# Kernel optimization log

Measured on AMD Instinct MI355X. Metric: run time of the kernel, lower is better.

Reference implementation:

```python
import jax, jax.numpy as jnp
import numpy as np

NOISE_DIM = 32
HIDDEN_DIM = 256
DATA_DIM = 2
TEMP = 0.05
N = 16384
DIAG_PENALTY = 1e6


def _cdist(a, b):
    # Euclidean pairwise distance [Na, Nb], safe sqrt (zero grad at d==0 like torch.cdist)
    d2 = (jnp.sum(a * a, -1)[:, None] + jnp.sum(b * b, -1)[None, :]
          - 2.0 * (a @ b.T))
    d2 = jnp.maximum(d2, 0.0)
    safe = jnp.where(d2 > 0, d2, 1.0)
    return jnp.where(d2 > 0, jnp.sqrt(safe), 0.0)


def setup_inputs() -> dict:
    key = jax.random.key(0)
    ks = jax.random.split(key, 12)
    pos = jax.random.normal(ks[0], (N, DATA_DIM), dtype=jnp.float32)
    z = jax.random.normal(ks[1], (N, NOISE_DIM), dtype=jnp.float32)
    def lin(k, fan_in, fan_out):
        bound = 1.0 / np.sqrt(fan_in)
        k1, k2 = jax.random.split(k)
        W = jax.random.uniform(k1, (fan_in, fan_out), minval=-bound, maxval=bound, dtype=jnp.float32)
        b = jax.random.uniform(k2, (fan_out,), minval=-bound, maxval=bound, dtype=jnp.float32)
        return W, b
    W1, b1 = lin(ks[2], NOISE_DIM, HIDDEN_DIM)
    W2, b2 = lin(ks[3], HIDDEN_DIM, HIDDEN_DIM)
    W3, b3 = lin(ks[4], HIDDEN_DIM, HIDDEN_DIM)
    W4, b4 = lin(ks[5], HIDDEN_DIM, HIDDEN_DIM)
    W5, b5 = lin(ks[6], HIDDEN_DIM, DATA_DIM)
    return {"pos": pos, "z": z, "W1": W1, "b1": b1, "W2": W2, "b2": b2,
            "W3": W3, "b3": b3, "W4": W4, "b4": b4, "W5": W5, "b5": b5}


def reference(pos, z, W1, b1, W2, b2, W3, b3, W4, b4, W5, b5):
    # SELU MLP generator
    h = jax.nn.selu(z @ W1 + b1)
    h = jax.nn.selu(h @ W2 + b2)
    h = jax.nn.selu(h @ W3 + b3)
    h = jax.nn.selu(h @ W4 + b4)
    gen = h @ W5 + b5  # [N, D]

    y_pos = jax.lax.stop_gradient(pos)
    y_neg = jax.lax.stop_gradient(gen)

    dist_pos = _cdist(gen, y_pos)  # [N, N]
    dist_neg = _cdist(gen, y_neg)  # [N, N]
    dist_neg = dist_neg + jnp.eye(gen.shape[0], dtype=gen.dtype) * DIAG_PENALTY

    energy_pos = -TEMP * jax.nn.logsumexp(-dist_pos / TEMP, axis=1)
    energy_neg = TEMP * jax.nn.logsumexp(-dist_neg / TEMP, axis=1)
    return energy_pos + energy_neg  # [N]
```

## Files before the change

kernel.cpp:

```cpp
#include <hip/hip_runtime.h>
#include <hip/hip_bf16.h>

#define N_PTS 16384
#define TEMP_F 0.05f

__device__ __forceinline__ float selu_f(float x) {
    const float scale = 1.0507009873554805f;
    const float alpha = 1.6732632423543772f;
    return x > 0.f ? scale * x : scale * alpha * (__expf(x) - 1.f);
}

__device__ __forceinline__ float fast_sqrtf(float x) {
#if __has_builtin(__builtin_amdgcn_sqrtf)
    return __builtin_amdgcn_sqrtf(x);
#else
    return sqrtf(x);
#endif
}

__device__ __forceinline__ float fast_exp2f(float x) {
#if __has_builtin(__builtin_amdgcn_exp2f)
    return __builtin_amdgcn_exp2f(x);
#else
    return exp2f(x);
#endif
}

__device__ __forceinline__ float fast_log2f(float x) {
#if __has_builtin(__builtin_amdgcn_logf)
    return __builtin_amdgcn_logf(x);
#else
    return log2f(x);
#endif
}

__global__ __launch_bounds__(1024) void mlp_kernel(
    const float* __restrict__ z,
    const float* __restrict__ W1, const float* __restrict__ b1,
    const float* __restrict__ W2, const float* __restrict__ b2,
    const float* __restrict__ W3, const float* __restrict__ b3,
    const float* __restrict__ W4, const float* __restrict__ b4,
    const float* __restrict__ W5, const float* __restrict__ b5,
    float* __restrict__ gen)
{
    __shared__ float h[256 * 64];

    const int t = threadIdx.x;
    const int r = t & 63;
    const int w = __builtin_amdgcn_readfirstlane(t >> 6);
    const int c0 = w * 16;
    const int row0 = blockIdx.x * 64;

    #pragma unroll
    for (int e = 0; e < 2; e++) {
        int f  = t + e * 1024;
        int rz = f >> 5;
        int kz = f & 31;
        h[kz * 64 + rz] = z[(row0 + rz) * 32 + kz];
    }
    __syncthreads();

    float acc[16];

    #pragma unroll
    for (int j = 0; j < 16; j++) acc[j] = b1[c0 + j];
    #pragma unroll 8
    for (int k = 0; k < 32; k++) {
        float hv = h[k * 64 + r];
        const float* Wr = W1 + k * 256 + c0;
        #pragma unroll
        for (int j = 0; j < 16; j++) acc[j] = fmaf(hv, Wr[j], acc[j]);
    }
    __syncthreads();
    #pragma unroll
    for (int j = 0; j < 16; j++) h[(c0 + j) * 64 + r] = selu_f(acc[j]);
    __syncthreads();

    for (int layer = 0; layer < 3; layer++) {
        const float* W = (layer == 0) ? W2 : (layer == 1) ? W3 : W4;
        const float* b = (layer == 0) ? b2 : (layer == 1) ? b3 : b4;
        #pragma unroll
        for (int j = 0; j < 16; j++) acc[j] = b[c0 + j];
        #pragma unroll 4
        for (int k = 0; k < 256; k++) {
            float hv = h[k * 64 + r];
            const float* Wr = W + k * 256 + c0;
            #pragma unroll
            for (int j = 0; j < 16; j++) acc[j] = fmaf(hv, Wr[j], acc[j]);
        }
        __syncthreads();
        #pragma unroll
        for (int j = 0; j < 16; j++) h[(c0 + j) * 64 + r] = selu_f(acc[j]);
        __syncthreads();
    }

    float p0 = 0.f, p1 = 0.f;
    #pragma unroll
    for (int kk = 0; kk < 16; kk++) {
        int k = c0 + kk;
        float hv = h[k * 64 + r];
        p0 = fmaf(hv, W5[k * 2 + 0], p0);
        p1 = fmaf(hv, W5[k * 2 + 1], p1);
    }
    __syncthreads();
    h[(0 * 16 + w) * 64 + r] = p0;
    h[(1 * 16 + w) * 64 + r] = p1;
    __syncthreads();
    if (t < 128) {
        int d  = t >> 6;
        int rr = t & 63;
        float sum = b5[d];
        #pragma unroll
        for (int ss = 0; ss < 16; ss++) sum += h[(d * 16 + ss) * 64 + rr];
        gen[(row0 + rr) * 2 + d] = sum;
    }
}

__global__ __launch_bounds__(512) void energy_kernel(
    const float* __restrict__ gen,
    const float* __restrict__ pos,
    float* __restrict__ out)
{
    __shared__ float4 sp[512];
    __shared__ float4 sg[512];

    const int t  = threadIdx.x;
    const int s  = t & 31;
    const int rl = t >> 5;
    const int i  = blockIdx.x * 16 + rl;
    const int diagBase = ((blockIdx.x * 16) >> 10) << 10;

    const float2 q = ((const float2*)gen)[i];

    const float cL2 = 28.853900817779268f;
    const float Tl2 = 0.034657359027997264f;
    const float cB  = 57.707801635558536f;

    float p0 = 0.f, p1 = 0.f, n0 = 0.f, n1 = 0.f;

    for (int base = 0; base < N_PTS; base += 1024) {
        __syncthreads();
        sp[t] = ((const float4*)pos)[base / 2 + t];
        sg[t] = ((const float4*)gen)[base / 2 + t];
        __syncthreads();
        if (base == diagBase) {
            #pragma unroll 4
            for (int u = 0; u < 16; u++) {
                int j = base + 2 * (s + 32 * u);
                float4 pp = sp[s + 32 * u];
                float4 gg = sg[s + 32 * u];
                float dx = q.x - pp.x, dy = q.y - pp.y;
                float d  = fast_sqrtf(fmaf(dx, dx, dy * dy));
                p0 += fast_exp2f(fmaf(-cL2, d, cB));
                dx = q.x - pp.z; dy = q.y - pp.w;
                d  = fast_sqrtf(fmaf(dx, dx, dy * dy));
                p1 += fast_exp2f(fmaf(-cL2, d, cB));
                dx = q.x - gg.x; dy = q.y - gg.y;
                d  = fast_sqrtf(fmaf(dx, dx, dy * dy));
                float e0 = fast_exp2f(fmaf(-cL2, d, cB));
                n0 += (j == i) ? 0.f : e0;
                dx = q.x - gg.z; dy = q.y - gg.w;
                d  = fast_sqrtf(fmaf(dx, dx, dy * dy));
                float e1 = fast_exp2f(fmaf(-cL2, d, cB));
                n1 += (j + 1 == i) ? 0.f : e1;
            }
        } else {
            #pragma unroll 4
            for (int u = 0; u < 16; u++) {
                float4 pp = sp[s + 32 * u];
                float4 gg = sg[s + 32 * u];
                float dx = q.x - pp.x, dy = q.y - pp.y;
                float d  = fast_sqrtf(fmaf(dx, dx, dy * dy));
                p0 += fast_exp2f(fmaf(-cL2, d, cB));
                dx = q.x - pp.z; dy = q.y - pp.w;
                d  = fast_sqrtf(fmaf(dx, dx, dy * dy));
                p1 += fast_exp2f(fmaf(-cL2, d, cB));
                dx = q.x - gg.x; dy = q.y - gg.y;
                d  = fast_sqrtf(fmaf(dx, dx, dy * dy));
                n0 += fast_exp2f(fmaf(-cL2, d, cB));
                dx = q.x - gg.z; dy = q.y - gg.w;
                d  = fast_sqrtf(fmaf(dx, dx, dy * dy));
                n1 += fast_exp2f(fmaf(-cL2, d, cB));
            }
        }
    }

    float sump = p0 + p1;
    float sumn = n0 + n1;
    #pragma unroll
    for (int m = 1; m < 32; m <<= 1) {
        sump += __shfl_xor(sump, m, 32);
        sumn += __shfl_xor(sumn, m, 32);
    }

    if (s == 0) {
        out[i] = Tl2 * (fast_log2f(sumn) - fast_log2f(sump));
    }
}

extern "C" void kernel_launch(void* const* d_in, const int* in_sizes, int n_in,
                              void* d_out, int out_size, void* d_ws, size_t ws_size,
                              hipStream_t stream) {
    const float* pos = (const float*)d_in[0];
    const float* z   = (const float*)d_in[1];
    const float* W1  = (const float*)d_in[2];
    const float* b1  = (const float*)d_in[3];
    const float* W2  = (const float*)d_in[4];
    const float* b2  = (const float*)d_in[5];
    const float* W3  = (const float*)d_in[6];
    const float* b3  = (const float*)d_in[7];
    const float* W4  = (const float*)d_in[8];
    const float* b4  = (const float*)d_in[9];
    const float* W5  = (const float*)d_in[10];
    const float* b5  = (const float*)d_in[11];

    float* gen = (float*)d_ws;

    mlp_kernel<<<N_PTS / 64, 1024, 0, stream>>>(z, W1, b1, W2, b2, W3, b3,
                                                W4, b4, W5, b5, gen);
    energy_kernel<<<N_PTS / 16, 512, 0, stream>>>(gen, pos, (float*)d_out);
}
```

Baseline: 291.5 us.

## Run MLP layers on bf16 MFMA with split hi/lo emulation of fp32

Replaces the scalar-FMA MLP kernel with a matrix-core kernel that splits each fp32 value into high and low bf16 parts and uses three MFMA products to approximate fp32 accuracy. A pack kernel, run on every call, reorders and splits the weights into MFMA fragment layout in workspace, and activations are kept in swizzled LDS as hi/lo bf16. This targets the FLOP-bound MLP, which the energy kernel follows. In exchange it adds an extra launch and carries some precision risk from dropping the lo*lo term. The old kernel remains only as a fallback when the workspace is too small.

```diff
diff --git a/kernel.cpp b/kernel.cpp
--- a/kernel.cpp
+++ b/kernel.cpp
@@ -3,6 +3,9 @@
 
 #define N_PTS 16384
 #define TEMP_F 0.05f
+
+typedef __attribute__((ext_vector_type(8))) short bf16x8;
+typedef __attribute__((ext_vector_type(4))) float f32x4;
 
 __device__ __forceinline__ float selu_f(float x) {
     const float scale = 1.0507009873554805f;
@@ -32,6 +35,185 @@
 #else
     return log2f(x);
 #endif
+}
+
+__device__ __forceinline__ f32x4 mfma_bf16(bf16x8 a, bf16x8 b, f32x4 c) {
+    return __builtin_amdgcn_mfma_f32_16x16x32_bf16(a, b, c, 0, 0, 0);
+}
+
+__device__ __forceinline__ void split_bf16(float v, unsigned short& hi, unsigned short& lo) {
+    unsigned u = __float_as_uint(v);
+    hi = (unsigned short)(u >> 16);
+    float ah = __uint_as_float(u & 0xFFFF0000u);
+    lo = (unsigned short)(__float_as_uint(v - ah) >> 16);
+}
+
+__global__ __launch_bounds__(512) void pack_kernel(
+    const float* __restrict__ W1, const float* __restrict__ W2,
+    const float* __restrict__ W3, const float* __restrict__ W4,
+    unsigned short* __restrict__ pk)
+{
+    int idx = blockIdx.x * 512 + threadIdx.x;
+    if (idx >= 204800) return;
+    const float* src;
+    unsigned short *dh, *dl;
+    int rem, kc, nt;
+    if (idx < 8192) {
+        src = W1; dh = pk; dl = pk + 8192;
+        rem = idx;
+        int g = rem >> 9;
+        kc = 0; nt = g;
+    } else {
+        int t2 = idx - 8192;
+        int ly = t2 >> 16;
+        rem = t2 & 65535;
+        src = (ly == 0) ? W2 : (ly == 1) ? W3 : W4;
+        dh = pk + 16384 + ly * 131072;
+        dl = dh + 65536;
+        int g = rem >> 9;
+        kc = g & 7; nt = g >> 3;
+    }
+    int e = rem & 7;
+    int l = (rem >> 3) & 63;
+    int n = nt * 16 + (l & 15);
+    int k = kc * 32 + ((l >> 4) << 3) + e;
+    float v = src[k * 256 + n];
+    unsigned short hb, lb;
+    split_bf16(v, hb, lb);
+    dh[rem] = hb;
+    dl[rem] = lb;
+}
+
+__global__ __launch_bounds__(512, 4) void mlp_mfma_kernel(
+    const float* __restrict__ z,
+    const unsigned short* __restrict__ pk,
+    const float* __restrict__ b1, const float* __restrict__ b2,
+    const float* __restrict__ b3, const float* __restrict__ b4,
+    const float* __restrict__ W5, const float* __restrict__ b5,
+    float* __restrict__ gen)
+{
+    __shared__ __align__(16) unsigned short Hh[64 * 256];
+    __shared__ __align__(16) unsigned short Hl[64 * 256];
+
+    const int t  = threadIdx.x;
+    const int l  = t & 63;
+    const int wv = t >> 6;
+    const int rt = wv >> 1;
+    const int ch = wv & 1;
+    const int lr = l & 15;
+    const int lq = l >> 4;
+    const int row0 = blockIdx.x * 64;
+    const int arow = rt * 16 + lr;
+
+    {
+        const float* zp = z + (row0 + arow) * 32 + lq * 8;
+        f32x4 z0 = *(const f32x4*)(zp);
+        f32x4 z1 = *(const f32x4*)(zp + 4);
+        bf16x8 ahf, alf;
+        #pragma unroll
+        for (int e = 0; e < 8; e++) {
+            float v = (e < 4) ? z0[e] : z1[e - 4];
+            unsigned short hb, lb;
+            split_bf16(v, hb, lb);
+            ahf[e] = (short)hb; alf[e] = (short)lb;
+        }
+        const bf16x8* B1h = (const bf16x8*)(pk);
+        const bf16x8* B1l = (const bf16x8*)(pk + 8192);
+        f32x4 acc[8];
+        #pragma unroll
+        for (int tile = 0; tile < 8; tile++) {
+            float bv = b1[ch * 128 + tile * 16 + lr];
+            acc[tile] = (f32x4){bv, bv, bv, bv};
+        }
+        #pragma unroll
+        for (int tile = 0; tile < 8; tile++) {
+            int nt = ch * 8 + tile;
+            bf16x8 bh = B1h[nt * 64 + l];
+            bf16x8 bl = B1l[nt * 64 + l];
+            acc[tile] = mfma_bf16(ahf, bh, acc[tile]);
+            acc[tile] = mfma_bf16(ahf, bl, acc[tile]);
+            acc[tile] = mfma_bf16(alf, bh, acc[tile]);
+        }
+        #pragma unroll
+        for (int tile = 0; tile < 8; tile++) {
+            #pragma unroll
+            for (int r = 0; r < 4; r++) {
+                float v = selu_f(acc[tile][r]);
+                int rowo = rt * 16 + lq * 4 + r;
+                int n = ch * 128 + tile * 16 + lr;
+                int o = (2 * n) ^ ((rowo & 7) << 4);
+                unsigned short hb, lb;
+                split_bf16(v, hb, lb);
+                Hh[rowo * 256 + (o >> 1)] = hb;
+                Hl[rowo * 256 + (o >> 1)] = lb;
+            }
+        }
+    }
+    __syncthreads();
+
+    #pragma unroll 1
+    for (int ly = 0; ly < 3; ly++) {
+        const unsigned short* wbase = pk + 16384 + ly * 131072;
+        const bf16x8* Bh = (const bf16x8*)(wbase);
+        const bf16x8* Bl = (const bf16x8*)(wbase + 65536);
+        const float* bb = (ly == 0) ? b2 : (ly == 1) ? b3 : b4;
+        f32x4 acc[8];
+        #pragma unroll
+        for (int tile = 0; tile < 8; tile++) {
+            float bv = bb[ch * 128 + tile * 16 + lr];
+            acc[tile] = (f32x4){bv, bv, bv, bv};
+        }
+        #pragma unroll 2
+        for (int kc = 0; kc < 8; kc++) {
+            int o = (kc * 64 + lq * 16) ^ ((arow & 7) << 4);
+            bf16x8 ahf = *(const bf16x8*)(Hh + arow * 256 + (o >> 1));
+            bf16x8 alf = *(const bf16x8*)(Hl + arow * 256 + (o >> 1));
+            #pragma unroll
+            for (int tile = 0; tile < 8; tile++) {
+                int nt = ch * 8 + tile;
+                bf16x8 bh = Bh[(nt * 8 + kc) * 64 + l];
+                bf16x8 bl = Bl[(nt * 8 + kc) * 64 + l];
+                acc[tile] = mfma_bf16(ahf, bh, acc[tile]);
+                acc[tile] = mfma_bf16(ahf, bl, acc[tile]);
+                acc[tile] = mfma_bf16(alf, bh, acc[tile]);
+            }
+        }
+        __syncthreads();
+        #pragma unroll
+        for (int tile = 0; tile < 8; tile++) {
+            #pragma unroll
+            for (int r = 0; r < 4; r++) {
+                float v = selu_f(acc[tile][r]);
+                int rowo = rt * 16 + lq * 4 + r;
+                int n = ch * 128 + tile * 16 + lr;
+                int o = (2 * n) ^ ((rowo & 7) << 4);
+                unsigned short hb, lb;
+                split_bf16(v, hb, lb);
+                Hh[rowo * 256 + (o >> 1)] = hb;
+                Hl[rowo * 256 + (o >> 1)] = lb;
+            }
+        }
+        __syncthreads();
+    }
+
+    if (t < 128) {
+        int row = t & 63;
+        int d = t >> 6;
+        float sum = b5[d];
+        #pragma unroll 4
+        for (int k = 0; k < 256; k += 8) {
+            int o = (2 * k) ^ ((row & 7) << 4);
+            bf16x8 hh = *(const bf16x8*)(Hh + row * 256 + (o >> 1));
+            bf16x8 ll = *(const bf16x8*)(Hl + row * 256 + (o >> 1));
+            #pragma unroll
+            for (int e = 0; e < 8; e++) {
+                float hv = __uint_as_float(((unsigned)(unsigned short)hh[e]) << 16)
+                         + __uint_as_float(((unsigned)(unsigned short)ll[e]) << 16);
+                sum = fmaf(hv, W5[(k + e) * 2 + d], sum);
+            }
+        }
+        gen[(row0 + row) * 2 + d] = sum;
+    }
 }
 
 __global__ __launch_bounds__(1024) void mlp_kernel(
@@ -215,8 +397,16 @@
     const float* b5  = (const float*)d_in[11];
 
     float* gen = (float*)d_ws;
-
-    mlp_kernel<<<N_PTS / 64, 1024, 0, stream>>>(z, W1, b1, W2, b2, W3, b3,
-                                                W4, b4, W5, b5, gen);
+    unsigned short* pk = (unsigned short*)((char*)d_ws + 131072);
+    const size_t WS_NEEDED = 131072 + (size_t)409600 * 2;
+
+    if (ws_size >= WS_NEEDED) {
+        pack_kernel<<<400, 512, 0, stream>>>(W1, W2, W3, W4, pk);
+        mlp_mfma_kernel<<<N_PTS / 64, 512, 0, stream>>>(z, pk, b1, b2, b3, b4,
+                                                        W5, b5, gen);
+    } else {
+        mlp_kernel<<<N_PTS / 64, 1024, 0, stream>>>(z, W1, b1, W2, b2, W3, b3,
+                                                    W4, b4, W5, b5, gen);
+    }
     energy_kernel<<<N_PTS / 16, 512, 0, stream>>>(gen, pos, (float*)d_out);
 }
```

Measured after the change: 275.7 us. -5.4%, faster.
